# Performance work log

Hardware: AMD Instinct MI355X
Metric: run time of the kernel (lower is better)

The kernel has to match this reference:

```python
import jax, jax.numpy as jnp
import numpy as np

D = 512
H = 512


def setup_inputs() -> dict:
    key = jax.random.key(0)
    k1, k2, k3, k4 = jax.random.split(key, 4)
    x = jax.random.normal(k1, (64, 512, D), dtype=jnp.float32)
    h0 = jax.random.normal(k2, (64, H), dtype=jnp.float32)
    Wx = jax.random.normal(k3, (D, 4 * H), dtype=jnp.float32) / jnp.sqrt(jnp.float32(D))
    Wh = jax.random.normal(k4, (H, 4 * H), dtype=jnp.float32) / jnp.sqrt(jnp.float32(H))
    b = jnp.zeros((4 * H,), dtype=jnp.float32)
    return {"x": x, "h0": h0, "Wx": Wx, "Wh": Wh, "b": b}


def reference(x, h0, Wx, Wh, b):
    # x: (N,T,D), h0: (N,H). Precompute input projection in one big GEMM.
    Hdim = h0.shape[1]
    xW = jnp.einsum('ntd,dk->ntk', x, Wx) + b  # (N,T,4H)
    c0 = jnp.zeros_like(h0)

    def step(carry, xw_t):
        prev_h, prev_c = carry
        a = xw_t + prev_h @ Wh  # (N,4H)
        i = jax.nn.sigmoid(a[:, 0:Hdim])
        f = jax.nn.sigmoid(a[:, Hdim:2 * Hdim])
        o = jax.nn.sigmoid(a[:, 2 * Hdim:3 * Hdim])
        g = jnp.tanh(a[:, 3 * Hdim:])
        next_c = f * prev_c + i * g
        next_h = o * jnp.tanh(next_c)
        return (next_h, next_c), next_h

    xW_t = jnp.swapaxes(xW, 0, 1)  # (T,N,4H) for scan
    _, hs = jax.lax.scan(step, (h0, c0), xW_t)
    return jnp.swapaxes(hs, 0, 1)  # (N,T,H)
```

## Files before the change

### kernel.cpp

```cpp
#include <hip/hip_runtime.h>

#define TSTEPS 512
#define DK 512
#define NC 2048
#define TB 4

typedef unsigned int u32;
typedef unsigned short u16;
typedef _Float16 f16x8 __attribute__((ext_vector_type(8)));
typedef __attribute__((ext_vector_type(4))) float f32x4;
typedef __attribute__((ext_vector_type(4))) unsigned int u32x4;
typedef __attribute__((ext_vector_type(2))) unsigned int u32x2;

static __device__ __forceinline__ u16 f2h(float f) {
    _Float16 h = (_Float16)f;
    u16 u; __builtin_memcpy(&u, &h, 2); return u;
}
static __device__ __forceinline__ float h2f(u16 u) {
    _Float16 h; __builtin_memcpy(&h, &u, 2); return (float)h;
}
static __device__ __forceinline__ u16 f2bf(float f) {
    u32 u = __float_as_uint(f);
    u += 0x7fffu + ((u >> 16) & 1u);
    return (u16)(u >> 16);
}
static __device__ __forceinline__ float sigmoidf_(float x) { return 1.0f / (1.0f + __expf(-x)); }
static __device__ __forceinline__ float tanhf_(float x)    { return 1.0f - 2.0f / (__expf(2.0f * x) + 1.0f); }

static __device__ __forceinline__ int fragaddr(int k, int n) {
    return ((k >> 5) << 9) + ((n | (((k >> 3) & 3) << 4)) << 3) + (k & 7);
}

static __device__ __forceinline__ void st_u16_sys(u16* p, u16 v) {
    asm volatile("global_store_short %0, %1, off sc0 sc1"
                 :: "v"(p), "v"((u32)v) : "memory");
}
static __device__ __forceinline__ void st_u32_sys(u32* p, u32 v) {
    asm volatile("global_store_dword %0, %1, off sc0 sc1"
                 :: "v"(p), "v"(v) : "memory");
}
static __device__ __forceinline__ u32 ld_u32_sys(const u32* p) {
    u32 v;
    asm volatile("global_load_dword %0, %1, off sc0 sc1\n\t"
                 "s_waitcnt vmcnt(0)"
                 : "=v"(v) : "v"(p) : "memory");
    return v;
}

__global__ __launch_bounds__(256)
void gemm_xwt_f16(const float* __restrict__ x, const float* __restrict__ Wx,
                  const float* __restrict__ bias, u16* __restrict__ xwt) {
    __shared__ __align__(16) u16 xF[8192];
    const int tid  = threadIdx.x;
    const int lane = tid & 63;
    const int wv   = __builtin_amdgcn_readfirstlane(tid >> 6);
    const int bid  = (int)blockIdx.x;
    const int tt   = bid >> 5;
    const int cb   = bid & 31;
    const int c0   = cb << 6;

    f16x8 Bf[16];
    const int coln = c0 + wv * 16 + (lane & 15);
    {
        #pragma unroll
        for (int K0 = 0; K0 < 16; ++K0) {
            f16x8 bv;
            #pragma unroll
            for (int jj = 0; jj < 8; ++jj) {
                const int k = K0 * 32 + ((lane >> 4) << 3) + jj;
                bv[jj] = (_Float16)Wx[(size_t)k * NC + coln];
            }
            Bf[K0] = bv;
        }
    }
    const float bi = bias[coln];

    const int n  = tid >> 4;
    const int q0 = (tid & 15) << 2;

    for (int ts = 0; ts < TB; ++ts) {
        const int t = tt * TB + ts;
        for (int bt = 0; bt < 4; ++bt) {
            const float* xp = x + ((size_t)(bt * 16 + n) * TSTEPS + t) * DK;
            __syncthreads();
            #pragma unroll
            for (int kq = 0; kq < 8; ++kq) {
                const int k = q0 + kq * 64;
                const float4 xv = *(const float4*)(xp + k);
                const u16 h0_ = f2h(xv.x), h1_ = f2h(xv.y);
                const u16 h2_ = f2h(xv.z), h3_ = f2h(xv.w);
                const int fa = fragaddr(k, n);
                u32x2 ph;
                ph[0] = (u32)h0_ | ((u32)h1_ << 16);
                ph[1] = (u32)h2_ | ((u32)h3_ << 16);
                *(u32x2*)&xF[fa] = ph;
            }
            __syncthreads();

            f32x4 acc = {0.f, 0.f, 0.f, 0.f};
            #pragma unroll
            for (int K0 = 0; K0 < 16; ++K0) {
                const f16x8 av = *(const f16x8*)&xF[K0 * 512 + lane * 8];
                acc = __builtin_amdgcn_mfma_f32_16x16x32_f16(av, Bf[K0], acc, 0, 0, 0);
            }

            const u16 s0 = f2h(acc[0] + bi);
            const u16 s1 = f2h(acc[1] + bi);
            const u16 s2 = f2h(acc[2] + bi);
            const u16 s3 = f2h(acc[3] + bi);
            u32x2 sv;
            sv[0] = (u32)s0 | ((u32)s1 << 16);
            sv[1] = (u32)s2 | ((u32)s3 << 16);
            const size_t row = (size_t)t * NC + coln;
            *(u32x2*)(xwt + row * 64 + bt * 16 + ((lane >> 4) << 2)) = sv;
        }
    }
}

__global__ __launch_bounds__(256)
void gemm_xw(const float* __restrict__ x, const float* __restrict__ Wx,
             const float* __restrict__ bias, u16* __restrict__ xw_out) {
    __shared__ float As[16][68];
    __shared__ float Bs[16][64];
    const int tid  = threadIdx.x;
    const int tx   = tid & 15;
    const int ty   = tid >> 4;
    const int row0 = blockIdx.x * 64;
    const int col0 = blockIdx.y * 64;
    const int ar = tid >> 2;
    const int ak = (tid & 3) << 2;
    const int bk = tid >> 4;
    const int bc = (tid & 15) << 2;
    float acc[4][4] = {};
    for (int k0 = 0; k0 < DK; k0 += 16) {
        const float4 av = *(const float4*)(x  + (size_t)(row0 + ar) * DK + k0 + ak);
        const float4 bv = *(const float4*)(Wx + (size_t)(k0 + bk) * NC + col0 + bc);
        __syncthreads();
        As[ak + 0][ar] = av.x; As[ak + 1][ar] = av.y;
        As[ak + 2][ar] = av.z; As[ak + 3][ar] = av.w;
        *(float4*)&Bs[bk][bc] = bv;
        __syncthreads();
        #pragma unroll
        for (int k = 0; k < 16; ++k) {
            float a4[4], b4[4];
            *(float4*)a4 = *(const float4*)&As[k][ty << 2];
            *(float4*)b4 = *(const float4*)&Bs[k][tx << 2];
            #pragma unroll
            for (int i = 0; i < 4; ++i)
                #pragma unroll
                for (int j = 0; j < 4; ++j)
                    acc[i][j] += a4[i] * b4[j];
        }
    }
    #pragma unroll
    for (int i = 0; i < 4; ++i) {
        const size_t row = (size_t)row0 + (ty << 2) + i;
        const int    col = col0 + (tx << 2);
        ushort4 s;
        s.x = f2bf(acc[i][0] + bias[col + 0]);
        s.y = f2bf(acc[i][1] + bias[col + 1]);
        s.z = f2bf(acc[i][2] + bias[col + 2]);
        s.w = f2bf(acc[i][3] + bias[col + 3]);
        *(ushort4*)(xw_out + row * NC + col) = s;
    }
}

static __device__ __forceinline__ float bf2f(u16 u) {
    return __uint_as_float(((u32)u) << 16);
}

__global__ __launch_bounds__(512)
void lstm_rec_old(const u16* __restrict__ xw, const float* __restrict__ Wh,
                  const float* __restrict__ h0, float* __restrict__ out) {
    __shared__ float h_s[DK];
    __shared__ float c_s[DK];
    __shared__ float a_s[NC];
    const int b   = blockIdx.x;
    const int tid = threadIdx.x;
    const int q   = tid << 2;
    h_s[tid] = h0[(size_t)b * DK + tid];
    c_s[tid] = 0.0f;
    __syncthreads();
    for (int t = 0; t < TSTEPS; ++t) {
        const size_t rowoff = ((size_t)b * TSTEPS + t) * NC;
        const ushort4 xv = *(const ushort4*)(xw + rowoff + q);
        float4 acc;
        acc.x = bf2f(xv.x); acc.y = bf2f(xv.y); acc.z = bf2f(xv.z); acc.w = bf2f(xv.w);
        const float* wp = Wh + q;
        #pragma unroll 4
        for (int k = 0; k < DK; k += 4) {
            const float4 hk = *(const float4*)&h_s[k];
            const float4 w0 = *(const float4*)(wp + (size_t)(k + 0) * NC);
            const float4 w1 = *(const float4*)(wp + (size_t)(k + 1) * NC);
            const float4 w2 = *(const float4*)(wp + (size_t)(k + 2) * NC);
            const float4 w3 = *(const float4*)(wp + (size_t)(k + 3) * NC);
            acc.x += hk.x * w0.x + hk.y * w1.x + hk.z * w2.x + hk.w * w3.x;
            acc.y += hk.x * w0.y + hk.y * w1.y + hk.z * w2.y + hk.w * w3.y;
            acc.z += hk.x * w0.z + hk.y * w1.z + hk.z * w2.z + hk.w * w3.z;
            acc.w += hk.x * w0.w + hk.y * w1.w + hk.z * w2.w + hk.w * w3.w;
        }
        *(float4*)&a_s[q] = acc;
        __syncthreads();
        const float ig = sigmoidf_(a_s[tid]);
        const float fg = sigmoidf_(a_s[DK + tid]);
        const float og = sigmoidf_(a_s[2 * DK + tid]);
        const float gg = tanhf_(a_s[3 * DK + tid]);
        const float c  = fg * c_s[tid] + ig * gg;
        const float h  = og * tanhf_(c);
        c_s[tid] = c;
        h_s[tid] = h;
        out[((size_t)b * TSTEPS + t) * DK + tid] = h;
        __syncthreads();
    }
}

__global__ void init_flg(u32* flg) {
    const int i = threadIdx.x;
    if (i < 128) flg[i] = 0u;
}

__global__ __launch_bounds__(256, 1)
void lstm_rec10(const u16* __restrict__ xwt, const float* __restrict__ Wh,
                const float* __restrict__ h0, float* __restrict__ out,
                u16* __restrict__ hG, u32* flg) {
    __shared__ __align__(16) u16 hF[8192];
    __shared__ float Cx[4][16][17];
    __shared__ float hT[256];
    __shared__ int deadS;

    const int tid  = threadIdx.x;
    const int lane = tid & 63;
    const int wv   = __builtin_amdgcn_readfirstlane(tid >> 6);
    const int g    = blockIdx.x;
    const int j    = g & 31;
    const int i    = g >> 5;
    const int du   = tid >> 4;
    const int bp   = tid & 15;
    const int u    = 16 * j + du;
    const int b    = 16 * i + bp;

    if (tid == 0) deadS = 0;

    {
        const float h0v = h0[(size_t)b * DK + u];
        u16* dst = hG + ((size_t)0 * 4 + i) * 8192;
        st_u16_sys(dst + fragaddr(u, bp), f2h(h0v));
    }
    float creg = 0.0f;
    __syncthreads();
    if (tid == 0) st_u32_sys(&flg[(i << 5) + j], 1u);

    f16x8 Bf[16];
    {
        const int coln = 16 * j + (lane & 15);
        #pragma unroll
        for (int K0 = 0; K0 < 16; ++K0) {
            f16x8 bv;
            #pragma unroll
            for (int jj = 0; jj < 8; ++jj) {
                const int k = K0 * 32 + ((lane >> 4) << 3) + jj;
                bv[jj] = (_Float16)Wh[(size_t)k * NC + wv * 512 + coln];
            }
            Bf[K0] = bv;
        }
    }

    const u32* fp = &flg[(i << 5) + (lane & 31)];

    for (int t = 0; t < TSTEPS; ++t) {
        const u16* xp = xwt + (size_t)t * (NC * 64);
        const u16 x0 = xp[(0 * 512 + u) * 64 + b];
        const u16 x1 = xp[(1 * 512 + u) * 64 + b];
        const u16 x2 = xp[(2 * 512 + u) * 64 + b];
        const u16 x3 = xp[(3 * 512 + u) * 64 + b];

        {
            const u32 target = (u32)(t + 1);
            int spins = 0;
            while (true) {
                const u32 v = ld_u32_sys(fp);
                if (__all((int)(v >= target))) break;
                if (++spins > (1 << 18)) { if (lane == 0) deadS = 1; break; }
                __builtin_amdgcn_s_sleep(1);
            }
        }

        {
            const char* srcb = (const char*)(hG + ((size_t)(t & 1) * 4 + i) * 8192);
            const char* p0 = srcb + (size_t)tid * 16;
            u32x4 q0, q1, q2, q3;
            asm volatile("global_load_dwordx4 %0, %1, off sc0 sc1" : "=v"(q0) : "v"(p0));
            asm volatile("global_load_dwordx4 %0, %1, off sc0 sc1" : "=v"(q1) : "v"(p0 + 4096));
            asm volatile("global_load_dwordx4 %0, %1, off sc0 sc1" : "=v"(q2) : "v"(p0 + 8192));
            asm volatile("global_load_dwordx4 %0, %1, off sc0 sc1" : "=v"(q3) : "v"(p0 + 12288));
            asm volatile("s_waitcnt vmcnt(0)" ::: "memory");
            __builtin_amdgcn_sched_barrier(0);
            u32* d32 = (u32*)&hF[0];
            *(u32x4*)(d32 + 0 * 1024 + tid * 4) = q0;
            *(u32x4*)(d32 + 1 * 1024 + tid * 4) = q1;
            *(u32x4*)(d32 + 2 * 1024 + tid * 4) = q2;
            *(u32x4*)(d32 + 3 * 1024 + tid * 4) = q3;
        }
        __syncthreads();
        if (deadS) break;

        f32x4 acc = {0.f, 0.f, 0.f, 0.f};
        #pragma unroll
        for (int K0 = 0; K0 < 16; ++K0) {
            const f16x8 ah = *(const f16x8*)&hF[K0 * 512 + lane * 8];
            acc = __builtin_amdgcn_mfma_f32_16x16x32_f16(ah, Bf[K0], acc, 0, 0, 0);
        }

        #pragma unroll
        for (int r = 0; r < 4; ++r)
            Cx[wv][lane & 15][((lane >> 4) << 2) + r] = acc[r];
        __syncthreads();

        const float ai = Cx[0][du][bp] + h2f(x0);
        const float af = Cx[1][du][bp] + h2f(x1);
        const float ao = Cx[2][du][bp] + h2f(x2);
        const float ag = Cx[3][du][bp] + h2f(x3);
        const float ig = sigmoidf_(ai);
        const float fg = sigmoidf_(af);
        const float og = sigmoidf_(ao);
        const float gg = tanhf_(ag);
        creg = fg * creg + ig * gg;
        const float hnew = og * tanhf_(creg);

        {
            u16* dst = hG + ((size_t)((t + 1) & 1) * 4 + i) * 8192;
            st_u16_sys(dst + fragaddr(u, bp), f2h(hnew));
        }
        hT[tid] = hnew;
        __syncthreads();

        if (tid == 0) st_u32_sys(&flg[(i << 5) + j], (u32)(t + 2));

        if (wv == 0) {
            const int bq = lane >> 2;
            const int qd = lane & 3;
            float4 o4;
            o4.x = hT[(qd * 4 + 0) * 16 + bq];
            o4.y = hT[(qd * 4 + 1) * 16 + bq];
            o4.z = hT[(qd * 4 + 2) * 16 + bq];
            o4.w = hT[(qd * 4 + 3) * 16 + bq];
            *(float4*)(out + ((size_t)(16 * i + bq) * TSTEPS + t) * DK + 16 * j + qd * 4) = o4;
        }
    }
}

extern "C" void kernel_launch(void* const* d_in, const int* in_sizes, int n_in,
                              void* d_out, int out_size, void* d_ws, size_t ws_size,
                              hipStream_t stream) {
    const float* x    = (const float*)d_in[0];
    const float* h0   = (const float*)d_in[1];
    const float* Wx   = (const float*)d_in[2];
    const float* Wh   = (const float*)d_in[3];
    const float* bias = (const float*)d_in[4];
    float* out = (float*)d_out;

    u16* xw = (u16*)d_ws;
    const size_t XW_BYTES = (size_t)TSTEPS * NC * 64 * sizeof(u16);
    u16* hG  = (u16*)((char*)d_ws + XW_BYTES);
    u32* flg = (u32*)((char*)d_ws + XW_BYTES + 262144);
    const size_t need = XW_BYTES + 262144 + 512;

    if (ws_size >= need) {
        gemm_xwt_f16<<<(TSTEPS / TB) * 32, 256, 0, stream>>>(x, Wx, bias, xw);
        init_flg<<<1, 128, 0, stream>>>(flg);
        lstm_rec10<<<128, 256, 0, stream>>>(xw, Wh, h0, out, hG, flg);
    } else {
        dim3 g1(512, 32);
        gemm_xw<<<g1, 256, 0, stream>>>(x, Wx, bias, xw);
        lstm_rec_old<<<64, 512, 0, stream>>>(xw, Wh, h0, out);
    }
}
```

Before: 1.467 ms.

## Use per-wave u16 flags and shuffle-based gate exchange in LSTM recurrence

Each wave now owns a column set that holds all four gates of its units, so the gate values are regathered with lane shuffles instead of an LDS transpose and an extra barrier. Each wave publishes its own 16-bit readiness flag right after storing h, instead of waiting for a block-wide barrier and a single-thread flag store. The output tile is also transposed through shuffles, the MFMA chain is split into two accumulators, and the input GEMM time-blocking TB rises from 4 to 8. This is meant to shorten the per-step critical path, at the cost of more spin polling on packed flags and a changed workspace offset for the flags.

```diff
diff --git a/kernel.cpp b/kernel.cpp
--- a/kernel.cpp
+++ b/kernel.cpp
@@ -3,7 +3,7 @@
 #define TSTEPS 512
 #define DK 512
 #define NC 2048
-#define TB 4
+#define TB 8
 
 typedef unsigned int u32;
 typedef unsigned short u16;
@@ -34,10 +34,6 @@
 static __device__ __forceinline__ void st_u16_sys(u16* p, u16 v) {
     asm volatile("global_store_short %0, %1, off sc0 sc1"
                  :: "v"(p), "v"((u32)v) : "memory");
-}
-static __device__ __forceinline__ void st_u32_sys(u32* p, u32 v) {
-    asm volatile("global_store_dword %0, %1, off sc0 sc1"
-                 :: "v"(p), "v"(v) : "memory");
 }
 static __device__ __forceinline__ u32 ld_u32_sys(const u32* p) {
     u32 v;
@@ -216,16 +212,14 @@
 
 __global__ void init_flg(u32* flg) {
     const int i = threadIdx.x;
-    if (i < 128) flg[i] = 0u;
+    if (i < 256) flg[i] = 0u;
 }
 
 __global__ __launch_bounds__(256, 1)
-void lstm_rec10(const u16* __restrict__ xwt, const float* __restrict__ Wh,
+void lstm_rec11(const u16* __restrict__ xwt, const float* __restrict__ Wh,
                 const float* __restrict__ h0, float* __restrict__ out,
-                u16* __restrict__ hG, u32* flg) {
+                u16* __restrict__ hG, u16* flg16) {
     __shared__ __align__(16) u16 hF[8192];
-    __shared__ float Cx[4][16][17];
-    __shared__ float hT[256];
     __shared__ int deadS;
 
     const int tid  = threadIdx.x;
@@ -234,9 +228,11 @@
     const int g    = blockIdx.x;
     const int j    = g & 31;
     const int i    = g >> 5;
-    const int du   = tid >> 4;
-    const int bp   = tid & 15;
-    const int u    = 16 * j + du;
+    const int p    = (lane >> 2) & 3;
+    const int q    = lane & 3;
+    const int rg   = lane >> 4;
+    const int u    = 16 * j + 4 * wv + p;
+    const int bp   = 4 * rg + q;
     const int b    = 16 * i + bp;
 
     if (tid == 0) deadS = 0;
@@ -245,41 +241,42 @@
         const float h0v = h0[(size_t)b * DK + u];
         u16* dst = hG + ((size_t)0 * 4 + i) * 8192;
         st_u16_sys(dst + fragaddr(u, bp), f2h(h0v));
+        asm volatile("s_waitcnt vmcnt(0)" ::: "memory");
+        if (lane == 0) st_u16_sys(flg16 + (i << 7) + (j << 2) + wv, (u16)1);
     }
     float creg = 0.0f;
-    __syncthreads();
-    if (tid == 0) st_u32_sys(&flg[(i << 5) + j], 1u);
 
     f16x8 Bf[16];
     {
-        const int coln = 16 * j + (lane & 15);
+        const int coln = q * 512 + 16 * j + 4 * wv + p;
         #pragma unroll
         for (int K0 = 0; K0 < 16; ++K0) {
             f16x8 bv;
             #pragma unroll
             for (int jj = 0; jj < 8; ++jj) {
                 const int k = K0 * 32 + ((lane >> 4) << 3) + jj;
-                bv[jj] = (_Float16)Wh[(size_t)k * NC + wv * 512 + coln];
+                bv[jj] = (_Float16)Wh[(size_t)k * NC + coln];
             }
             Bf[K0] = bv;
         }
     }
 
-    const u32* fp = &flg[(i << 5) + (lane & 31)];
+    const u32* fp = (const u32*)flg16 + (i << 6) + lane;
 
     for (int t = 0; t < TSTEPS; ++t) {
         const u16* xp = xwt + (size_t)t * (NC * 64);
-        const u16 x0 = xp[(0 * 512 + u) * 64 + b];
-        const u16 x1 = xp[(1 * 512 + u) * 64 + b];
-        const u16 x2 = xp[(2 * 512 + u) * 64 + b];
-        const u16 x3 = xp[(3 * 512 + u) * 64 + b];
+        const u16 x0 = xp[(size_t)(0 * 512 + u) * 64 + b];
+        const u16 x1 = xp[(size_t)(1 * 512 + u) * 64 + b];
+        const u16 x2 = xp[(size_t)(2 * 512 + u) * 64 + b];
+        const u16 x3 = xp[(size_t)(3 * 512 + u) * 64 + b];
 
         {
             const u32 target = (u32)(t + 1);
             int spins = 0;
             while (true) {
                 const u32 v = ld_u32_sys(fp);
-                if (__all((int)(v >= target))) break;
+                const int ok = ((v & 0xffffu) >= target) && ((v >> 16) >= target);
+                if (__all(ok)) break;
                 if (++spins > (1 << 18)) { if (lane == 0) deadS = 1; break; }
                 __builtin_amdgcn_s_sleep(1);
             }
@@ -304,48 +301,61 @@
         __syncthreads();
         if (deadS) break;
 
-        f32x4 acc = {0.f, 0.f, 0.f, 0.f};
+        f32x4 acc0 = {0.f, 0.f, 0.f, 0.f};
+        f32x4 acc1 = {0.f, 0.f, 0.f, 0.f};
         #pragma unroll
-        for (int K0 = 0; K0 < 16; ++K0) {
-            const f16x8 ah = *(const f16x8*)&hF[K0 * 512 + lane * 8];
-            acc = __builtin_amdgcn_mfma_f32_16x16x32_f16(ah, Bf[K0], acc, 0, 0, 0);
-        }
-
-        #pragma unroll
-        for (int r = 0; r < 4; ++r)
-            Cx[wv][lane & 15][((lane >> 4) << 2) + r] = acc[r];
-        __syncthreads();
-
-        const float ai = Cx[0][du][bp] + h2f(x0);
-        const float af = Cx[1][du][bp] + h2f(x1);
-        const float ao = Cx[2][du][bp] + h2f(x2);
-        const float ag = Cx[3][du][bp] + h2f(x3);
-        const float ig = sigmoidf_(ai);
-        const float fg = sigmoidf_(af);
-        const float og = sigmoidf_(ao);
-        const float gg = tanhf_(ag);
+        for (int K0 = 0; K0 < 16; K0 += 2) {
+            const f16x8 a0 = *(const f16x8*)&hF[(K0 + 0) * 512 + lane * 8];
+            const f16x8 a1 = *(const f16x8*)&hF[(K0 + 1) * 512 + lane * 8];
+            acc0 = __builtin_amdgcn_mfma_f32_16x16x32_f16(a0, Bf[K0 + 0], acc0, 0, 0, 0);
+            acc1 = __builtin_amdgcn_mfma_f32_16x16x32_f16(a1, Bf[K0 + 1], acc1, 0, 0, 0);
+        }
+        const f32x4 a = acc0 + acc1;
+
+        f32x4 tsw, bv, ssw, cv;
+        tsw[0] = __shfl_xor(a[0], 1); tsw[1] = __shfl_xor(a[1], 1);
+        tsw[2] = __shfl_xor(a[2], 1); tsw[3] = __shfl_xor(a[3], 1);
+        bv[0] = (q & 1) ? tsw[1] : a[0];
+        bv[1] = (q & 1) ? a[1]   : tsw[0];
+        bv[2] = (q & 1) ? tsw[3] : a[2];
+        bv[3] = (q & 1) ? a[3]   : tsw[2];
+        ssw[0] = __shfl_xor(bv[0], 2); ssw[1] = __shfl_xor(bv[1], 2);
+        ssw[2] = __shfl_xor(bv[2], 2); ssw[3] = __shfl_xor(bv[3], 2);
+        cv[0] = (q & 2) ? ssw[2] : bv[0];
+        cv[1] = (q & 2) ? ssw[3] : bv[1];
+        cv[2] = (q & 2) ? bv[2]  : ssw[0];
+        cv[3] = (q & 2) ? bv[3]  : ssw[1];
+
+        const float ig = sigmoidf_(cv[0] + h2f(x0));
+        const float fg = sigmoidf_(cv[1] + h2f(x1));
+        const float og = sigmoidf_(cv[2] + h2f(x2));
+        const float gg = tanhf_   (cv[3] + h2f(x3));
         creg = fg * creg + ig * gg;
         const float hnew = og * tanhf_(creg);
 
         {
             u16* dst = hG + ((size_t)((t + 1) & 1) * 4 + i) * 8192;
             st_u16_sys(dst + fragaddr(u, bp), f2h(hnew));
-        }
-        hT[tid] = hnew;
-        __syncthreads();
-
-        if (tid == 0) st_u32_sys(&flg[(i << 5) + j], (u32)(t + 2));
-
-        if (wv == 0) {
-            const int bq = lane >> 2;
-            const int qd = lane & 3;
+            asm volatile("s_waitcnt vmcnt(0)" ::: "memory");
+            if (lane == 0)
+                st_u16_sys(flg16 + (i << 7) + (j << 2) + wv, (u16)(t + 2));
+        }
+
+        {
+            const float g4 = __shfl_xor(hnew, 4);
+            const float e0 = (p & 1) ? g4 : hnew;
+            const float e1 = (p & 1) ? hnew : g4;
+            const float f0 = __shfl_xor(e0, 8);
+            const float f1 = __shfl_xor(e1, 8);
             float4 o4;
-            o4.x = hT[(qd * 4 + 0) * 16 + bq];
-            o4.y = hT[(qd * 4 + 1) * 16 + bq];
-            o4.z = hT[(qd * 4 + 2) * 16 + bq];
-            o4.w = hT[(qd * 4 + 3) * 16 + bq];
-            *(float4*)(out + ((size_t)(16 * i + bq) * TSTEPS + t) * DK + 16 * j + qd * 4) = o4;
-        }
+            o4.x = (p & 2) ? f0 : e0;
+            o4.y = (p & 2) ? f1 : e1;
+            o4.z = (p & 2) ? e0 : f0;
+            o4.w = (p & 2) ? e1 : f1;
+            if (p == 0)
+                *(float4*)(out + ((size_t)b * TSTEPS + t) * DK + 16 * j + 4 * wv) = o4;
+        }
+        __syncthreads();
     }
 }
 
@@ -362,13 +372,13 @@
     u16* xw = (u16*)d_ws;
     const size_t XW_BYTES = (size_t)TSTEPS * NC * 64 * sizeof(u16);
     u16* hG  = (u16*)((char*)d_ws + XW_BYTES);
-    u32* flg = (u32*)((char*)d_ws + XW_BYTES + 262144);
+    u16* flg = (u16*)((char*)d_ws + XW_BYTES + 200704);
     const size_t need = XW_BYTES + 262144 + 512;
 
     if (ws_size >= need) {
         gemm_xwt_f16<<<(TSTEPS / TB) * 32, 256, 0, stream>>>(x, Wx, bias, xw);
-        init_flg<<<1, 128, 0, stream>>>(flg);
-        lstm_rec10<<<128, 256, 0, stream>>>(xw, Wh, h0, out, hG, flg);
+        init_flg<<<1, 256, 0, stream>>>((u32*)flg);
+        lstm_rec11<<<128, 256, 0, stream>>>(xw, Wh, h0, out, hG, flg);
     } else {
         dim3 g1(512, 32);
         gemm_xw<<<g1, 256, 0, stream>>>(x, Wx, bias, xw);
```

New measurement: 2.060 ms. +40.5%, slower.
